# Performance work log

Hardware: AMD Instinct MI355X
Metric: run time of the kernel (lower is better)

Reference implementation:

```python
import jax, jax.numpy as jnp
import numpy as np

Q_HEADS, KV_HEADS, DIMS, IN_DIMS = 16, 4, 1024, 1024
HEAD_D = DIMS // Q_HEADS            # 64
GROUPS = Q_HEADS // KV_HEADS        # 4
ROPE_BASE = 10000.0


def nd_rope(x, coords):
    """N-D rotary embedding.
    x: [..., s, d]; coords: broadcastable [..., s, a] (float).
    Head dim d is split into a contiguous chunks of d//a; within each chunk
    consecutive pairs (2i, 2i+1) are rotated by angle coord_axis * base^(-2i/(d//a)).
    """
    a = coords.shape[-1]
    d = x.shape[-1]
    dpa = d // a                                  # dims per coordinate axis (even)
    inv_freq = ROPE_BASE ** (-jnp.arange(dpa // 2, dtype=jnp.float32) * (2.0 / dpa))
    angles = coords[..., :, None] * inv_freq      # [..., s, a, dpa//2]
    angles = angles.reshape(angles.shape[:-2] + (d // 2,))
    cos, sin = jnp.cos(angles), jnp.sin(angles)
    xp = x.reshape(x.shape[:-1] + (d // 2, 2))
    x1, x2 = xp[..., 0], xp[..., 1]
    return jnp.stack([x1 * cos - x2 * sin, x1 * sin + x2 * cos], axis=-1).reshape(x.shape)


def setup_inputs() -> dict:
    key = jax.random.key(0)
    k1, k2, k3, k4, k5, k6, k7, k8 = jax.random.split(key, 8)
    B, SQ, SKV, A = 4, 2048, 2048, 2
    q = jax.random.normal(k1, (B, SQ, IN_DIMS), dtype=jnp.float32)
    kv = jax.random.normal(k2, (B, SKV, IN_DIMS), dtype=jnp.float32)
    q_coords = jax.random.randint(k3, (B, SQ, A), 0, 2048, dtype=jnp.int32)
    kv_coords = jax.random.randint(k4, (B, SKV, A), 0, 2048, dtype=jnp.int32)
    s_in = 1.0 / np.sqrt(IN_DIMS)
    Wq = jax.random.normal(k5, (IN_DIMS, Q_HEADS, HEAD_D), dtype=jnp.float32) * s_in
    Wk = jax.random.normal(k6, (IN_DIMS, KV_HEADS, HEAD_D), dtype=jnp.float32) * s_in
    Wv = jax.random.normal(k7, (IN_DIMS, KV_HEADS, HEAD_D), dtype=jnp.float32) * s_in
    Wo = jax.random.normal(k8, (KV_HEADS * HEAD_D, IN_DIMS), dtype=jnp.float32) * (1.0 / np.sqrt(KV_HEADS * HEAD_D))
    return {"q": q, "q_coords": q_coords, "kv": kv, "kv_coords": kv_coords,
            "Wq": Wq, "Wk": Wk, "Wv": Wv, "Wo": Wo}


def reference(q, q_coords, kv, kv_coords, Wq, Wk, Wv, Wo):
    B, SQ = q.shape[0], q.shape[1]
    qp = jnp.einsum('bsi,ihd->bshd', q, Wq)   # [b, sq, q_heads, hd]
    kp = jnp.einsum('bsi,ihd->bshd', kv, Wk)  # [b, skv, kv_heads, hd]
    vp = jnp.einsum('bsi,ihd->bshd', kv, Wv)
    # '... s (h g) d -> ... g h s d' with h=KV_HEADS outer, g=GROUPS inner
    qp = qp.reshape(B, SQ, KV_HEADS, GROUPS, HEAD_D).transpose(0, 3, 2, 1, 4)  # [b,g,h,sq,hd]
    kp = kp.transpose(0, 2, 1, 3)  # [b,h,skv,hd]
    vp = vp.transpose(0, 2, 1, 3)
    qc = q_coords.astype(jnp.float32)[:, None, None]  # [b,1,1,sq,a] -> broadcast over g,h
    kc = kv_coords.astype(jnp.float32)[:, None]       # [b,1,skv,a] -> broadcast over h
    qr = nd_rope(qp, qc)
    kr = nd_rope(kp, kc)
    # NOTE: einops pattern omits g in output -> group axis is SUMMED (faithful to source)
    scores = jnp.einsum('bghsd,bhad->bhsa', qr, kr) / (HEAD_D ** 0.5)
    attn = jax.nn.softmax(scores, axis=-1)
    out = jnp.einsum('bhsa,bhad->bhsd', attn, vp)
    out = out.transpose(0, 2, 1, 3).reshape(B, SQ, KV_HEADS * HEAD_D)
    return out @ Wo
```

## Files before the change

### kernel.cpp

```cpp
#include <hip/hip_runtime.h>

#define BATCH 4
#define SEQQ  2048
#define SEQKV 2048
#define NH    4
#define HD    64
#define IND   1024
#define QSCL 0.18033688011112042f

typedef __attribute__((ext_vector_type(8))) short short8;
typedef __attribute__((ext_vector_type(4))) short s4v;
typedef __attribute__((ext_vector_type(4))) float floatx4;

#if defined(__HIP_DEVICE_COMPILE__) && __has_builtin(__builtin_amdgcn_exp2f)
  #define EXP2(x) __builtin_amdgcn_exp2f(x)
#else
  #define EXP2(x) exp2f(x)
#endif

#if defined(__HIP_DEVICE_COMPILE__)
  #if __has_builtin(__builtin_amdgcn_mfma_f32_16x16x16bf16_1k)
    #define MFMA16(a, b, c) __builtin_amdgcn_mfma_f32_16x16x16bf16_1k(a, b, c, 0, 0, 0)
  #elif __has_builtin(__builtin_amdgcn_mfma_f32_16x16x16_bf16)
    #define MFMA16(a, b, c) __builtin_amdgcn_mfma_f32_16x16x16_bf16(a, b, c, 0, 0, 0)
  #else
    #error "no 16x16x16 bf16 MFMA builtin on gfx950 device pass"
  #endif
#else
  #define MFMA16(a, b, c) (c)
#endif
#define MFMA32(a, b, c) __builtin_amdgcn_mfma_f32_16x16x32_bf16(a, b, c, 0, 0, 0)

__device__ __forceinline__ short f2b(float f) {
    unsigned u; __builtin_memcpy(&u, &f, 4);
    u = (u + 0x7fffu + ((u >> 16) & 1u)) >> 16;
    return (short)u;
}
__device__ __forceinline__ short8 cvt8(const float* p) {
    float4 a = *(const float4*)p;
    float4 b = *(const float4*)(p + 4);
    short8 r;
    r[0] = f2b(a.x); r[1] = f2b(a.y); r[2] = f2b(a.z); r[3] = f2b(a.w);
    r[4] = f2b(b.x); r[5] = f2b(b.y); r[6] = f2b(b.z); r[7] = f2b(b.w);
    return r;
}

__global__ __launch_bounds__(256) void prep_all(
    const float* __restrict__ Wq, const float* __restrict__ Wk,
    const float* __restrict__ Wv, const float* __restrict__ Wo,
    const float* __restrict__ q, const float* __restrict__ kv,
    short* __restrict__ Wq_t, short* __restrict__ Wkv_t, short* __restrict__ Wo_t,
    short* __restrict__ qb, short* __restrict__ kvb) {
    __shared__ short Ts[64][65];
    int blk = blockIdx.x;
    if (blk < 256) {
        int c4 = threadIdx.x & 63, r4 = threadIdx.x >> 6;
        if (blk < 64) {
            int h = blk & 3, ib = blk >> 2;
#pragma unroll 4
            for (int jj = 0; jj < 16; ++jj) {
                int il = r4 * 16 + jj;
                float s = 0.f;
#pragma unroll
                for (int g = 0; g < 4; ++g)
                    s += Wq[(ib * 64 + il) * 1024 + (h * 4 + g) * 64 + c4];
                Ts[il][c4] = f2b(s);
            }
            __syncthreads();
#pragma unroll 4
            for (int jj = 0; jj < 16; ++jj) {
                int dl = r4 * 16 + jj;
                Wq_t[(h * 64 + dl) * 1024 + ib * 64 + c4] = Ts[c4][dl];
            }
        } else if (blk < 192) {
            int t = blk - 64, ss = t >> 6; t &= 63;
            int ib = t >> 2, nb = t & 3;
            const float* W = ss ? Wv : Wk;
#pragma unroll 4
            for (int jj = 0; jj < 16; ++jj) {
                int il = r4 * 16 + jj;
                Ts[il][c4] = f2b(W[(ib * 64 + il) * 256 + nb * 64 + c4]);
            }
            __syncthreads();
#pragma unroll 4
            for (int jj = 0; jj < 16; ++jj) {
                int dl = r4 * 16 + jj;
                Wkv_t[(ss * 256 + nb * 64 + dl) * 1024 + ib * 64 + c4] = Ts[c4][dl];
            }
        } else {
            int t = blk - 192, kb = t >> 4, nb = t & 15;
#pragma unroll 4
            for (int jj = 0; jj < 16; ++jj) {
                int il = r4 * 16 + jj;
                Ts[il][c4] = f2b(Wo[(kb * 64 + il) * 1024 + nb * 64 + c4]);
            }
            __syncthreads();
#pragma unroll 4
            for (int jj = 0; jj < 16; ++jj) {
                int dl = r4 * 16 + jj;
                Wo_t[(nb * 64 + dl) * 256 + kb * 64 + c4] = Ts[c4][dl];
            }
        }
    } else if (blk < 2304) {
        long e = ((long)(blk - 256) * 256 + threadIdx.x) * 16;
        *(short8*)(qb + e)     = cvt8(q + e);
        *(short8*)(qb + e + 8) = cvt8(q + e + 8);
    } else {
        long e = ((long)(blk - 2304) * 256 + threadIdx.x) * 16;
        *(short8*)(kvb + e)     = cvt8(kv + e);
        *(short8*)(kvb + e + 8) = cvt8(kv + e + 8);
    }
}

template <int MODE>
__device__ __forceinline__ void gemm128(
    const short* __restrict__ A, const short* __restrict__ Wt,
    int m0, int n0, int N, int K, short* As, short* Bs,
    float* __restrict__ C, const int* __restrict__ coords,
    short* __restrict__ ropeDst, short* __restrict__ vDst) {
    const int t = threadIdx.x;
    const int w = t >> 6, lane = t & 63, ln = lane & 15, quad = lane >> 4;
    const int wm = w >> 1, wn = w & 1;
    const int srow = lane >> 2, skc = (lane & 3) * 8;
    floatx4 acc[4][4];
#pragma unroll
    for (int mt = 0; mt < 4; ++mt)
#pragma unroll
        for (int nt = 0; nt < 4; ++nt) acc[mt][nt] = floatx4{0.f, 0.f, 0.f, 0.f};

    auto stage = [&](int ks, int sel) {
#pragma unroll
        for (int i = 0; i < 2; ++i) {
            __builtin_amdgcn_global_load_lds(
                (const void*)(A + (long)(m0 + w * 32 + i * 16 + srow) * K + ks + skc),
                (void*)(As + sel * 4096 + (w * 2 + i) * 512), 16, 0, 0);
            __builtin_amdgcn_global_load_lds(
                (const void*)(Wt + (long)(n0 + w * 32 + i * 16 + srow) * K + ks + skc),
                (void*)(Bs + sel * 4096 + (w * 2 + i) * 512), 16, 0, 0);
        }
    };

    const int nk = K >> 5;
    stage(0, 0);
    __syncthreads();
    int cur = 0;
    for (int tt = 0; tt < nk; ++tt) {
        if (tt < nk - 1) stage((tt + 1) * 32, cur ^ 1);
        const short* Ac = As + cur * 4096;
        const short* Bc = Bs + cur * 4096;
        short8 af[4], bf[4];
#pragma unroll
        for (int mt = 0; mt < 4; ++mt)
            af[mt] = *(const short8*)(Ac + (wm * 64 + mt * 16 + ln) * 32 + quad * 8);
#pragma unroll
        for (int nt = 0; nt < 4; ++nt)
            bf[nt] = *(const short8*)(Bc + (wn * 64 + nt * 16 + ln) * 32 + quad * 8);
#pragma unroll
        for (int mt = 0; mt < 4; ++mt)
#pragma unroll
            for (int nt = 0; nt < 4; ++nt)
                acc[mt][nt] = MFMA32(af[mt], bf[nt], acc[mt][nt]);
        __syncthreads();
        cur ^= 1;
    }

    if (MODE == 0) {
#pragma unroll
        for (int mt = 0; mt < 4; ++mt) {
            int row0 = m0 + wm * 64 + mt * 16 + quad * 4;
#pragma unroll
            for (int nt = 0; nt < 4; ++nt) {
                int col = n0 + wn * 64 + nt * 16 + ln;
#pragma unroll
                for (int r = 0; r < 4; ++r)
                    C[(long)(row0 + r) * N + col] = acc[mt][nt][r];
            }
        }
    } else {
        const int wn_col = n0 + wn * 64;
        if (MODE == 1 || wn_col < 256) {
            const int h = (wn_col >> 6) & 3;
            const float scl = (MODE == 1) ? QSCL : 1.0f;
            const float L = -0.5756462732485114f;
            const float fA = __expf((float)(ln >> 1) * L);
            const float fB = __expf((float)(8 + (ln >> 1)) * L);
            const float sgn = (ln & 1) ? 1.0f : -1.0f;
#pragma unroll
            for (int mt = 0; mt < 4; ++mt) {
                int row0 = m0 + wm * 64 + mt * 16 + quad * 4;
#pragma unroll
                for (int r = 0; r < 4; ++r) {
                    int row = row0 + r;
                    float c0 = (float)coords[row * 2];
                    float c1 = (float)coords[row * 2 + 1];
                    float snv[4], csv[4];
                    __sincosf(c0 * fA, &snv[0], &csv[0]);
                    __sincosf(c0 * fB, &snv[1], &csv[1]);
                    __sincosf(c1 * fA, &snv[2], &csv[2]);
                    __sincosf(c1 * fB, &snv[3], &csv[3]);
                    long rbase = ((long)((row >> 11) * 4 + h) * 2048 + (row & 2047)) * 64;
#pragma unroll
                    for (int nt = 0; nt < 4; ++nt) {
                        float v = acc[mt][nt][r];
                        float p = __shfl_xor(v, 1, 64);
                        float o = v * (csv[nt] * scl) + p * (snv[nt] * (scl * sgn));
                        ropeDst[rbase + nt * 16 + ln] = f2b(o);
                    }
                }
            }
        } else {
            const int h = ((wn_col - 256) >> 6) & 3;
#pragma unroll
            for (int mt = 0; mt < 4; ++mt) {
                int row0 = m0 + wm * 64 + mt * 16 + quad * 4;
                int b = row0 >> 11, s0 = row0 & 2047;
#pragma unroll
                for (int nt = 0; nt < 4; ++nt) {
                    s4v ov;
#pragma unroll
                    for (int r = 0; r < 4; ++r) ov[r] = f2b(acc[mt][nt][r]);
                    *(s4v*)(vDst + (long)((b * 4 + h) * 64 + nt * 16 + ln) * 2048 + s0) = ov;
                }
            }
        }
    }
}

__global__ __launch_bounds__(256) void proj_gemm(
    const short* __restrict__ qb, const short* __restrict__ kvb,
    const short* __restrict__ Wq_t, const short* __restrict__ Wkv_t,
    const int* __restrict__ qc, const int* __restrict__ kvc,
    short* __restrict__ Qr, short* __restrict__ Kr, short* __restrict__ Vt) {
    __shared__ __align__(16) short As[2][128 * 32];
    __shared__ __align__(16) short Bs[2][128 * 32];
    int id = blockIdx.x;
    if (id < 128)
        gemm128<1>(qb, Wq_t, (id >> 1) * 128, (id & 1) * 128, 256, 1024,
                   &As[0][0], &Bs[0][0], nullptr, qc, Qr, nullptr);
    else {
        int t = id - 128;
        gemm128<2>(kvb, Wkv_t, (t >> 2) * 128, (t & 3) * 128, 512, 1024,
                   &As[0][0], &Bs[0][0], nullptr, kvc, Kr, Vt);
    }
}

__global__ __launch_bounds__(256) void final_gemm(
    const short* __restrict__ Ob, const short* __restrict__ Wo_t, float* __restrict__ out) {
    __shared__ __align__(16) short As[2][128 * 32];
    __shared__ __align__(16) short Bs[2][128 * 32];
    gemm128<0>(Ob, Wo_t, blockIdx.x * 128, blockIdx.y * 128, 1024, 256,
               &As[0][0], &Bs[0][0], out, nullptr, nullptr, nullptr);
}

__global__ __launch_bounds__(256, 4) void attn_kernel(
    const short* __restrict__ Qr, const short* __restrict__ Kr,
    const short* __restrict__ Vt, float* __restrict__ Op, float* __restrict__ Lp) {
    __shared__ __align__(16) short Kls[2][64 * 64];
    __shared__ __align__(16) short Vls[2][64 * 64];
    const int blk = blockIdx.x;
    const int bh = blk & 15, sp = (blk >> 4) & 3, qg = blk >> 6;
    const int w = threadIdx.x >> 6, lane = threadIdx.x & 63;
    const int ln = lane & 15, quad = lane >> 4;
    const int q0 = qg * 128 + w * 32;
    const short* Qb = Qr + (long)bh * SEQKV * HD;
    const short* Kb = Kr + (long)bh * SEQKV * HD;
    const short* Vb = Vt + (long)bh * HD * SEQKV;

    const int srow = lane >> 3;
    const int schk = (lane & 7) ^ (srow & 7);
    const long kstage0 = (long)(w * 16 + srow) * HD + schk * 8;
    const long vstage0 = (long)(w * 16 + srow) * SEQKV + schk * 8;

    short8 qf[2][2];
#pragma unroll
    for (int qs = 0; qs < 2; ++qs)
#pragma unroll
        for (int ck = 0; ck < 2; ++ck)
            qf[qs][ck] = *(const short8*)(Qb + (long)(q0 + qs * 16 + ln) * HD + ck * 32 + quad * 8);

    s4v ones;
#pragma unroll
    for (int j = 0; j < 4; ++j) ones[j] = (short)0x3F80;

    floatx4 o[2][4], ol[2];
#pragma unroll
    for (int qs = 0; qs < 2; ++qs) {
        ol[qs] = floatx4{0.f, 0.f, 0.f, 0.f};
#pragma unroll
        for (int nt = 0; nt < 4; ++nt) o[qs][nt] = floatx4{0.f, 0.f, 0.f, 0.f};
    }

    const int ln7 = ln & 7;
    int koff[2];
#pragma unroll
    for (int ck = 0; ck < 2; ++ck) koff[ck] = ln * 64 + ((ck * 4 + quad) ^ ln7) * 8;
    int voff[4];
#pragma unroll
    for (int t = 0; t < 4; ++t) voff[t] = ln * 64 + ((t * 2 + (quad >> 1)) ^ ln7) * 8 + (quad & 1) * 4;

    const int kt0 = sp * 512;
#define STAGE(kt, sel)                                                              \
    do {                                                                            \
        _Pragma("unroll")                                                           \
        for (int i = 0; i < 2; ++i) {                                               \
            __builtin_amdgcn_global_load_lds(                                       \
                (const void*)(Kb + (long)(kt) * HD + kstage0 + (long)i * 8 * HD),   \
                (void*)(Kls[sel] + (w * 16 + i * 8) * 64), 16, 0, 0);               \
            __builtin_amdgcn_global_load_lds(                                       \
                (const void*)(Vb + (kt) + vstage0 + (long)i * 8 * SEQKV),           \
                (void*)(Vls[sel] + (w * 16 + i * 8) * 64), 16, 0, 0);               \
        }                                                                           \
    } while (0)

    STAGE(kt0, 0);
    __syncthreads();
    int cur = 0;
    for (int tt = 0; tt < 8; ++tt) {
        if (tt < 7) STAGE(kt0 + (tt + 1) * 64, cur ^ 1);
        const short* Kc = Kls[cur];
        const short* Vc = Vls[cur];
#pragma unroll
        for (int t = 0; t < 4; ++t) {
            short8 a0 = *(const short8*)(Kc + t * 1024 + koff[0]);
            short8 a1 = *(const short8*)(Kc + t * 1024 + koff[1]);
            floatx4 st0 = {0.f, 0.f, 0.f, 0.f}, st1 = {0.f, 0.f, 0.f, 0.f};
            __builtin_amdgcn_s_setprio(1);
            st0 = MFMA32(a0, qf[0][0], st0);
            st1 = MFMA32(a0, qf[1][0], st1);
            st0 = MFMA32(a1, qf[0][1], st0);
            st1 = MFMA32(a1, qf[1][1], st1);
            __builtin_amdgcn_s_setprio(0);
            float e0 = EXP2(st0[0]), e1 = EXP2(st0[1]), e2 = EXP2(st0[2]), e3 = EXP2(st0[3]);
            float g0 = EXP2(st1[0]), g1 = EXP2(st1[1]), g2 = EXP2(st1[2]), g3 = EXP2(st1[3]);
            unsigned a0p, a1p, b0p, b1p;
            asm("v_cvt_pk_bf16_f32 %0, %1, %2" : "=v"(a0p) : "v"(e0), "v"(e1));
            asm("v_cvt_pk_bf16_f32 %0, %1, %2" : "=v"(a1p) : "v"(e2), "v"(e3));
            asm("v_cvt_pk_bf16_f32 %0, %1, %2" : "=v"(b0p) : "v"(g0), "v"(g1));
            asm("v_cvt_pk_bf16_f32 %0, %1, %2" : "=v"(b1p) : "v"(g2), "v"(g3));
            s4v pt0, pt1;
            { unsigned tmp[2] = {a0p, a1p}; __builtin_memcpy(&pt0, tmp, 8); }
            { unsigned tmp[2] = {b0p, b1p}; __builtin_memcpy(&pt1, tmp, 8); }
            __builtin_amdgcn_s_setprio(1);
#pragma unroll
            for (int nt = 0; nt < 4; ++nt) {
                s4v vf = *(const s4v*)(Vc + nt * 1024 + voff[t]);
                o[0][nt] = MFMA16(vf, pt0, o[0][nt]);
                o[1][nt] = MFMA16(vf, pt1, o[1][nt]);
            }
            ol[0] = MFMA16(ones, pt0, ol[0]);
            ol[1] = MFMA16(ones, pt1, ol[1]);
            __builtin_amdgcn_s_setprio(0);
        }
        __syncthreads();
        cur ^= 1;
    }
#undef STAGE
#pragma unroll
    for (int qs = 0; qs < 2; ++qs) {
        long qrow = (long)(sp * 16 + bh) * 2048 + q0 + qs * 16 + ln;
        if (quad == 0) Lp[qrow] = ol[qs][0];
#pragma unroll
        for (int nt = 0; nt < 4; ++nt)
            *(floatx4*)(Op + qrow * 64 + nt * 16 + quad * 4) = o[qs][nt];
    }
}

__global__ __launch_bounds__(256) void combine_kernel(
    const float* __restrict__ Op, const float* __restrict__ Lp, short* __restrict__ Ob) {
    int idx = blockIdx.x * 256 + threadIdx.x;
    int row = idx >> 4;
    int d0 = (idx & 15) * 4;
    int bh = row >> 11, qq = row & 2047;
    int b = bh >> 2, h = bh & 3;
    float4 os = {0.f, 0.f, 0.f, 0.f};
    float ls = 0.f;
#pragma unroll
    for (int s = 0; s < 4; ++s) {
        long rr = (long)(s * 16 + bh) * 2048 + qq;
        float4 v = *(const float4*)(Op + rr * 64 + d0);
        os.x += v.x; os.y += v.y; os.z += v.z; os.w += v.w;
        ls += Lp[rr];
    }
    float li = 1.f / ls;
    s4v ov;
    ov[0] = f2b(os.x * li); ov[1] = f2b(os.y * li);
    ov[2] = f2b(os.z * li); ov[3] = f2b(os.w * li);
    *(s4v*)(Ob + ((long)(b * 2048 + qq)) * 256 + h * 64 + d0) = ov;
}

extern "C" void kernel_launch(void* const* d_in, const int* in_sizes, int n_in,
                              void* d_out, int out_size, void* d_ws, size_t ws_size,
                              hipStream_t stream) {
    const float* q   = (const float*)d_in[0];
    const int*   qc  = (const int*)d_in[1];
    const float* kv  = (const float*)d_in[2];
    const int*   kvc = (const int*)d_in[3];
    const float* Wq  = (const float*)d_in[4];
    const float* Wk  = (const float*)d_in[5];
    const float* Wv  = (const float*)d_in[6];
    const float* Wo  = (const float*)d_in[7];
    float* out = (float*)d_out;

    char* ws = (char*)d_ws;
    const size_t MB = 1024 * 1024;
    short* Wq_t  = (short*)(ws);
    short* Wkv_t = (short*)(ws + MB / 2);
    short* Wo_t  = (short*)(ws + 3 * MB / 2);
    short* qb    = (short*)(ws + 2 * MB);
    short* kvb   = (short*)(ws + 18 * MB);
    short* Qr    = (short*)(ws + 34 * MB);
    short* Kr    = (short*)(ws + 38 * MB);
    short* Vt    = (short*)(ws + 42 * MB);
    short* Ob    = (short*)(ws + 46 * MB);
    float* Opart = (float*)(ws + 50 * MB);
    float* Lpart = (float*)(ws + 82 * MB);

    hipLaunchKernelGGL(prep_all, dim3(4352), dim3(256), 0, stream,
                       Wq, Wk, Wv, Wo, q, kv, Wq_t, Wkv_t, Wo_t, qb, kvb);
    hipLaunchKernelGGL(proj_gemm, dim3(384), dim3(256), 0, stream,
                       qb, kvb, Wq_t, Wkv_t, qc, kvc, Qr, Kr, Vt);
    hipLaunchKernelGGL(attn_kernel, dim3(1024), dim3(256), 0, stream,
                       Qr, Kr, Vt, Opart, Lpart);
    hipLaunchKernelGGL(combine_kernel, dim3(2048), dim3(256), 0, stream,
                       Opart, Lpart, Ob);
    hipLaunchKernelGGL(final_gemm, dim3(64, 8), dim3(256), 0, stream, Ob, Wo_t, out);
}
```

Baseline: 193.6 us.

## Fuse fp32 input conversion into projection GEMM and drop split-KV attention combine

The projection GEMM now stages the fp32 q/kv activations into LDS with an XOR swizzle and converts them to bf16 in registers. This removes the separate conversion pass that wrote bf16 copies of the inputs. The attention kernel no longer splits the KV range four ways. Each block covers 64 queries over the full 2048 keys, normalises in-kernel and writes bf16 output directly, which eliminates the partial-sum buffers and the combine kernel. The trade-offs are half as many attention blocks (512) with a longer serial loop, and a larger fp32 LDS footprint in the projection.

Measured after the change: 209.5 us. +8.2%, slower.

```diff
diff --git a/kernel.cpp b/kernel.cpp
--- a/kernel.cpp
+++ b/kernel.cpp
@@ -36,92 +36,73 @@
     u = (u + 0x7fffu + ((u >> 16) & 1u)) >> 16;
     return (short)u;
 }
-__device__ __forceinline__ short8 cvt8(const float* p) {
-    float4 a = *(const float4*)p;
-    float4 b = *(const float4*)(p + 4);
-    short8 r;
-    r[0] = f2b(a.x); r[1] = f2b(a.y); r[2] = f2b(a.z); r[3] = f2b(a.w);
-    r[4] = f2b(b.x); r[5] = f2b(b.y); r[6] = f2b(b.z); r[7] = f2b(b.w);
-    return r;
-}
-
-__global__ __launch_bounds__(256) void prep_all(
+
+__global__ __launch_bounds__(256) void prep_w(
     const float* __restrict__ Wq, const float* __restrict__ Wk,
     const float* __restrict__ Wv, const float* __restrict__ Wo,
-    const float* __restrict__ q, const float* __restrict__ kv,
-    short* __restrict__ Wq_t, short* __restrict__ Wkv_t, short* __restrict__ Wo_t,
-    short* __restrict__ qb, short* __restrict__ kvb) {
+    short* __restrict__ Wq_t, short* __restrict__ Wkv_t, short* __restrict__ Wo_t) {
     __shared__ short Ts[64][65];
     int blk = blockIdx.x;
-    if (blk < 256) {
-        int c4 = threadIdx.x & 63, r4 = threadIdx.x >> 6;
-        if (blk < 64) {
-            int h = blk & 3, ib = blk >> 2;
-#pragma unroll 4
-            for (int jj = 0; jj < 16; ++jj) {
-                int il = r4 * 16 + jj;
-                float s = 0.f;
-#pragma unroll
-                for (int g = 0; g < 4; ++g)
-                    s += Wq[(ib * 64 + il) * 1024 + (h * 4 + g) * 64 + c4];
-                Ts[il][c4] = f2b(s);
-            }
-            __syncthreads();
-#pragma unroll 4
-            for (int jj = 0; jj < 16; ++jj) {
-                int dl = r4 * 16 + jj;
-                Wq_t[(h * 64 + dl) * 1024 + ib * 64 + c4] = Ts[c4][dl];
-            }
-        } else if (blk < 192) {
-            int t = blk - 64, ss = t >> 6; t &= 63;
-            int ib = t >> 2, nb = t & 3;
-            const float* W = ss ? Wv : Wk;
-#pragma unroll 4
-            for (int jj = 0; jj < 16; ++jj) {
-                int il = r4 * 16 + jj;
-                Ts[il][c4] = f2b(W[(ib * 64 + il) * 256 + nb * 64 + c4]);
-            }
-            __syncthreads();
-#pragma unroll 4
-            for (int jj = 0; jj < 16; ++jj) {
-                int dl = r4 * 16 + jj;
-                Wkv_t[(ss * 256 + nb * 64 + dl) * 1024 + ib * 64 + c4] = Ts[c4][dl];
-            }
-        } else {
-            int t = blk - 192, kb = t >> 4, nb = t & 15;
-#pragma unroll 4
-            for (int jj = 0; jj < 16; ++jj) {
-                int il = r4 * 16 + jj;
-                Ts[il][c4] = f2b(Wo[(kb * 64 + il) * 1024 + nb * 64 + c4]);
-            }
-            __syncthreads();
-#pragma unroll 4
-            for (int jj = 0; jj < 16; ++jj) {
-                int dl = r4 * 16 + jj;
-                Wo_t[(nb * 64 + dl) * 256 + kb * 64 + c4] = Ts[c4][dl];
-            }
-        }
-    } else if (blk < 2304) {
-        long e = ((long)(blk - 256) * 256 + threadIdx.x) * 16;
-        *(short8*)(qb + e)     = cvt8(q + e);
-        *(short8*)(qb + e + 8) = cvt8(q + e + 8);
+    int c4 = threadIdx.x & 63, r4 = threadIdx.x >> 6;
+    if (blk < 64) {
+        int h = blk & 3, ib = blk >> 2;
+#pragma unroll 4
+        for (int jj = 0; jj < 16; ++jj) {
+            int il = r4 * 16 + jj;
+            float s = 0.f;
+#pragma unroll
+            for (int g = 0; g < 4; ++g)
+                s += Wq[(ib * 64 + il) * 1024 + (h * 4 + g) * 64 + c4];
+            Ts[il][c4] = f2b(s);
+        }
+        __syncthreads();
+#pragma unroll 4
+        for (int jj = 0; jj < 16; ++jj) {
+            int dl = r4 * 16 + jj;
+            Wq_t[(h * 64 + dl) * 1024 + ib * 64 + c4] = Ts[c4][dl];
+        }
+    } else if (blk < 192) {
+        int t = blk - 64, ss = t >> 6; t &= 63;
+        int ib = t >> 2, nb = t & 3;
+        const float* W = ss ? Wv : Wk;
+#pragma unroll 4
+        for (int jj = 0; jj < 16; ++jj) {
+            int il = r4 * 16 + jj;
+            Ts[il][c4] = f2b(W[(ib * 64 + il) * 256 + nb * 64 + c4]);
+        }
+        __syncthreads();
+#pragma unroll 4
+        for (int jj = 0; jj < 16; ++jj) {
+            int dl = r4 * 16 + jj;
+            Wkv_t[(ss * 256 + nb * 64 + dl) * 1024 + ib * 64 + c4] = Ts[c4][dl];
+        }
     } else {
-        long e = ((long)(blk - 2304) * 256 + threadIdx.x) * 16;
-        *(short8*)(kvb + e)     = cvt8(kv + e);
-        *(short8*)(kvb + e + 8) = cvt8(kv + e + 8);
+        int t = blk - 192, kb = t >> 4, nb = t & 15;
+#pragma unroll 4
+        for (int jj = 0; jj < 16; ++jj) {
+            int il = r4 * 16 + jj;
+            Ts[il][c4] = f2b(Wo[(kb * 64 + il) * 1024 + nb * 64 + c4]);
+        }
+        __syncthreads();
+#pragma unroll 4
+        for (int jj = 0; jj < 16; ++jj) {
+            int dl = r4 * 16 + jj;
+            Wo_t[(nb * 64 + dl) * 256 + kb * 64 + c4] = Ts[c4][dl];
+        }
     }
 }
 
 template <int MODE>
-__device__ __forceinline__ void gemm128(
-    const short* __restrict__ A, const short* __restrict__ Wt,
-    int m0, int n0, int N, int K, short* As, short* Bs,
-    float* __restrict__ C, const int* __restrict__ coords,
-    short* __restrict__ ropeDst, short* __restrict__ vDst) {
-    const int t = threadIdx.x;
-    const int w = t >> 6, lane = t & 63, ln = lane & 15, quad = lane >> 4;
+__device__ __forceinline__ void gemm128_f32(
+    const float* __restrict__ A, const short* __restrict__ Wt,
+    int m0, int n0, int K, float* Asf, short* Bs,
+    const int* __restrict__ coords, short* __restrict__ ropeDst,
+    short* __restrict__ vDst) {
+    const int tid = threadIdx.x;
+    const int w = tid >> 6, lane = tid & 63, ln = lane & 15, quad = lane >> 4;
     const int wm = w >> 1, wn = w & 1;
-    const int srow = lane >> 2, skc = (lane & 3) * 8;
+    const int srowA = lane >> 3, schkA = (lane & 7) ^ (srowA & 7);
+    const int srowB = lane >> 2, skcB = (lane & 3) * 8;
     floatx4 acc[4][4];
 #pragma unroll
     for (int mt = 0; mt < 4; ++mt)
@@ -130,14 +111,15 @@
 
     auto stage = [&](int ks, int sel) {
 #pragma unroll
-        for (int i = 0; i < 2; ++i) {
+        for (int i = 0; i < 4; ++i)
             __builtin_amdgcn_global_load_lds(
-                (const void*)(A + (long)(m0 + w * 32 + i * 16 + srow) * K + ks + skc),
-                (void*)(As + sel * 4096 + (w * 2 + i) * 512), 16, 0, 0);
+                (const void*)(A + (long)(m0 + w * 32 + i * 8 + srowA) * 1024 + ks + schkA * 4),
+                (void*)(Asf + sel * 4096 + (w * 32 + i * 8) * 32), 16, 0, 0);
+#pragma unroll
+        for (int i = 0; i < 2; ++i)
             __builtin_amdgcn_global_load_lds(
-                (const void*)(Wt + (long)(n0 + w * 32 + i * 16 + srow) * K + ks + skc),
+                (const void*)(Wt + (long)(n0 + w * 32 + i * 16 + srowB) * K + ks + skcB),
                 (void*)(Bs + sel * 4096 + (w * 2 + i) * 512), 16, 0, 0);
-        }
     };
 
     const int nk = K >> 5;
@@ -146,12 +128,23 @@
     int cur = 0;
     for (int tt = 0; tt < nk; ++tt) {
         if (tt < nk - 1) stage((tt + 1) * 32, cur ^ 1);
-        const short* Ac = As + cur * 4096;
+        const float* Ac = Asf + cur * 4096;
         const short* Bc = Bs + cur * 4096;
+        const int e = ln & 7;
         short8 af[4], bf[4];
 #pragma unroll
-        for (int mt = 0; mt < 4; ++mt)
-            af[mt] = *(const short8*)(Ac + (wm * 64 + mt * 16 + ln) * 32 + quad * 8);
+        for (int mt = 0; mt < 4; ++mt) {
+            const float* rp = Ac + (wm * 64 + mt * 16 + ln) * 32;
+            float4 lo = *(const float4*)(rp + ((2 * quad) ^ e) * 4);
+            float4 hi = *(const float4*)(rp + ((2 * quad + 1) ^ e) * 4);
+            unsigned p0, p1, p2, p3;
+            asm("v_cvt_pk_bf16_f32 %0, %1, %2" : "=v"(p0) : "v"(lo.x), "v"(lo.y));
+            asm("v_cvt_pk_bf16_f32 %0, %1, %2" : "=v"(p1) : "v"(lo.z), "v"(lo.w));
+            asm("v_cvt_pk_bf16_f32 %0, %1, %2" : "=v"(p2) : "v"(hi.x), "v"(hi.y));
+            asm("v_cvt_pk_bf16_f32 %0, %1, %2" : "=v"(p3) : "v"(hi.z), "v"(hi.w));
+            unsigned tmp[4] = {p0, p1, p2, p3};
+            __builtin_memcpy(&af[mt], tmp, 16);
+        }
 #pragma unroll
         for (int nt = 0; nt < 4; ++nt)
             bf[nt] = *(const short8*)(Bc + (wn * 64 + nt * 16 + ln) * 32 + quad * 8);
@@ -164,83 +157,69 @@
         cur ^= 1;
     }
 
-    if (MODE == 0) {
+    const int wn_col = n0 + wn * 64;
+    if (MODE == 1 || wn_col < 256) {
+        const int h = (wn_col >> 6) & 3;
+        const float scl = (MODE == 1) ? QSCL : 1.0f;
+        const float L = -0.5756462732485114f;
+        const float fA = __expf((float)(ln >> 1) * L);
+        const float fB = __expf((float)(8 + (ln >> 1)) * L);
+        const float sgn = (ln & 1) ? 1.0f : -1.0f;
 #pragma unroll
         for (int mt = 0; mt < 4; ++mt) {
             int row0 = m0 + wm * 64 + mt * 16 + quad * 4;
 #pragma unroll
-            for (int nt = 0; nt < 4; ++nt) {
-                int col = n0 + wn * 64 + nt * 16 + ln;
-#pragma unroll
-                for (int r = 0; r < 4; ++r)
-                    C[(long)(row0 + r) * N + col] = acc[mt][nt][r];
-            }
-        }
-    } else {
-        const int wn_col = n0 + wn * 64;
-        if (MODE == 1 || wn_col < 256) {
-            const int h = (wn_col >> 6) & 3;
-            const float scl = (MODE == 1) ? QSCL : 1.0f;
-            const float L = -0.5756462732485114f;
-            const float fA = __expf((float)(ln >> 1) * L);
-            const float fB = __expf((float)(8 + (ln >> 1)) * L);
-            const float sgn = (ln & 1) ? 1.0f : -1.0f;
-#pragma unroll
-            for (int mt = 0; mt < 4; ++mt) {
-                int row0 = m0 + wm * 64 + mt * 16 + quad * 4;
-#pragma unroll
-                for (int r = 0; r < 4; ++r) {
-                    int row = row0 + r;
-                    float c0 = (float)coords[row * 2];
-                    float c1 = (float)coords[row * 2 + 1];
-                    float snv[4], csv[4];
-                    __sincosf(c0 * fA, &snv[0], &csv[0]);
-                    __sincosf(c0 * fB, &snv[1], &csv[1]);
-                    __sincosf(c1 * fA, &snv[2], &csv[2]);
-                    __sincosf(c1 * fB, &snv[3], &csv[3]);
-                    long rbase = ((long)((row >> 11) * 4 + h) * 2048 + (row & 2047)) * 64;
-#pragma unroll
-                    for (int nt = 0; nt < 4; ++nt) {
-                        float v = acc[mt][nt][r];
-                        float p = __shfl_xor(v, 1, 64);
-                        float o = v * (csv[nt] * scl) + p * (snv[nt] * (scl * sgn));
-                        ropeDst[rbase + nt * 16 + ln] = f2b(o);
-                    }
+            for (int r = 0; r < 4; ++r) {
+                int row = row0 + r;
+                float c0 = (float)coords[row * 2];
+                float c1 = (float)coords[row * 2 + 1];
+                float snv[4], csv[4];
+                __sincosf(c0 * fA, &snv[0], &csv[0]);
+                __sincosf(c0 * fB, &snv[1], &csv[1]);
+                __sincosf(c1 * fA, &snv[2], &csv[2]);
+                __sincosf(c1 * fB, &snv[3], &csv[3]);
+                long rbase = ((long)((row >> 11) * 4 + h) * 2048 + (row & 2047)) * 64;
+#pragma unroll
+                for (int nt = 0; nt < 4; ++nt) {
+                    float v = acc[mt][nt][r];
+                    float p = __shfl_xor(v, 1, 64);
+                    float o = v * (csv[nt] * scl) + p * (snv[nt] * (scl * sgn));
+                    ropeDst[rbase + nt * 16 + ln] = f2b(o);
                 }
             }
-        } else {
-            const int h = ((wn_col - 256) >> 6) & 3;
-#pragma unroll
-            for (int mt = 0; mt < 4; ++mt) {
-                int row0 = m0 + wm * 64 + mt * 16 + quad * 4;
-                int b = row0 >> 11, s0 = row0 & 2047;
-#pragma unroll
-                for (int nt = 0; nt < 4; ++nt) {
-                    s4v ov;
-#pragma unroll
-                    for (int r = 0; r < 4; ++r) ov[r] = f2b(acc[mt][nt][r]);
-                    *(s4v*)(vDst + (long)((b * 4 + h) * 64 + nt * 16 + ln) * 2048 + s0) = ov;
-                }
+        }
+    } else {
+        const int h = ((wn_col - 256) >> 6) & 3;
+#pragma unroll
+        for (int mt = 0; mt < 4; ++mt) {
+            int row0 = m0 + wm * 64 + mt * 16 + quad * 4;
+            int b = row0 >> 11, s0 = row0 & 2047;
+#pragma unroll
+            for (int nt = 0; nt < 4; ++nt) {
+                s4v ov;
+#pragma unroll
+                for (int r = 0; r < 4; ++r) ov[r] = f2b(acc[mt][nt][r]);
+                *(s4v*)(vDst + (long)((b * 4 + h) * 64 + nt * 16 + ln) * 2048 + s0) = ov;
             }
         }
     }
 }
 
 __global__ __launch_bounds__(256) void proj_gemm(
-    const short* __restrict__ qb, const short* __restrict__ kvb,
+    const float* __restrict__ q, const float* __restrict__ kv,
     const short* __restrict__ Wq_t, const short* __restrict__ Wkv_t,
     const int* __restrict__ qc, const int* __restrict__ kvc,
     short* __restrict__ Qr, short* __restrict__ Kr, short* __restrict__ Vt) {
-    __shared__ __align__(16) short As[2][128 * 32];
-    __shared__ __align__(16) short Bs[2][128 * 32];
+    __shared__ __align__(16) float Asf[2 * 4096];
+    __shared__ __align__(16) short Bsb[2 * 4096];
     int id = blockIdx.x;
     if (id < 128)
-        gemm128<1>(qb, Wq_t, (id >> 1) * 128, (id & 1) * 128, 256, 1024,
-                   &As[0][0], &Bs[0][0], nullptr, qc, Qr, nullptr);
+        gemm128_f32<1>(q, Wq_t, (id >> 1) * 128, (id & 1) * 128, 1024,
+                       Asf, Bsb, qc, Qr, nullptr);
     else {
         int t = id - 128;
-        gemm128<2>(kvb, Wkv_t, (t >> 2) * 128, (t & 3) * 128, 512, 1024,
-                   &As[0][0], &Bs[0][0], nullptr, kvc, Kr, Vt);
+        gemm128_f32<2>(kv, Wkv_t, (t >> 2) * 128, (t & 3) * 128, 1024,
+                       Asf, Bsb, kvc, Kr, Vt);
     }
 }
 
@@ -248,20 +227,74 @@
     const short* __restrict__ Ob, const short* __restrict__ Wo_t, float* __restrict__ out) {
     __shared__ __align__(16) short As[2][128 * 32];
     __shared__ __align__(16) short Bs[2][128 * 32];
-    gemm128<0>(Ob, Wo_t, blockIdx.x * 128, blockIdx.y * 128, 1024, 256,
-               &As[0][0], &Bs[0][0], out, nullptr, nullptr, nullptr);
+    const int m0 = blockIdx.x * 128, n0 = blockIdx.y * 128;
+    const int tid = threadIdx.x;
+    const int w = tid >> 6, lane = tid & 63, ln = lane & 15, quad = lane >> 4;
+    const int wm = w >> 1, wn = w & 1;
+    const int srow = lane >> 2, skc = (lane & 3) * 8;
+    floatx4 acc[4][4];
+#pragma unroll
+    for (int mt = 0; mt < 4; ++mt)
+#pragma unroll
+        for (int nt = 0; nt < 4; ++nt) acc[mt][nt] = floatx4{0.f, 0.f, 0.f, 0.f};
+
+    auto stage = [&](int ks, int sel) {
+#pragma unroll
+        for (int i = 0; i < 2; ++i) {
+            __builtin_amdgcn_global_load_lds(
+                (const void*)(Ob + (long)(m0 + w * 32 + i * 16 + srow) * 256 + ks + skc),
+                (void*)(&As[sel][(w * 2 + i) * 512]), 16, 0, 0);
+            __builtin_amdgcn_global_load_lds(
+                (const void*)(Wo_t + (long)(n0 + w * 32 + i * 16 + srow) * 256 + ks + skc),
+                (void*)(&Bs[sel][(w * 2 + i) * 512]), 16, 0, 0);
+        }
+    };
+    stage(0, 0);
+    __syncthreads();
+    int cur = 0;
+    for (int tt = 0; tt < 8; ++tt) {
+        if (tt < 7) stage((tt + 1) * 32, cur ^ 1);
+        const short* Ac = &As[cur][0];
+        const short* Bc = &Bs[cur][0];
+        short8 af[4], bf[4];
+#pragma unroll
+        for (int mt = 0; mt < 4; ++mt)
+            af[mt] = *(const short8*)(Ac + (wm * 64 + mt * 16 + ln) * 32 + quad * 8);
+#pragma unroll
+        for (int nt = 0; nt < 4; ++nt)
+            bf[nt] = *(const short8*)(Bc + (wn * 64 + nt * 16 + ln) * 32 + quad * 8);
+#pragma unroll
+        for (int mt = 0; mt < 4; ++mt)
+#pragma unroll
+            for (int nt = 0; nt < 4; ++nt)
+                acc[mt][nt] = MFMA32(af[mt], bf[nt], acc[mt][nt]);
+        __syncthreads();
+        cur ^= 1;
+    }
+#pragma unroll
+    for (int mt = 0; mt < 4; ++mt) {
+        int row0 = m0 + wm * 64 + mt * 16 + quad * 4;
+#pragma unroll
+        for (int nt = 0; nt < 4; ++nt) {
+            int col = n0 + wn * 64 + nt * 16 + ln;
+#pragma unroll
+            for (int r = 0; r < 4; ++r)
+                out[(long)(row0 + r) * 1024 + col] = acc[mt][nt][r];
+        }
+    }
 }
 
 __global__ __launch_bounds__(256, 4) void attn_kernel(
     const short* __restrict__ Qr, const short* __restrict__ Kr,
-    const short* __restrict__ Vt, float* __restrict__ Op, float* __restrict__ Lp) {
+    const short* __restrict__ Vt, short* __restrict__ Ob) {
     __shared__ __align__(16) short Kls[2][64 * 64];
     __shared__ __align__(16) short Vls[2][64 * 64];
     const int blk = blockIdx.x;
-    const int bh = blk & 15, sp = (blk >> 4) & 3, qg = blk >> 6;
+    const int x = blk & 7, y = blk >> 3;
+    const int bh = x * 2 + (y >> 5), qg = y & 31;
     const int w = threadIdx.x >> 6, lane = threadIdx.x & 63;
     const int ln = lane & 15, quad = lane >> 4;
-    const int q0 = qg * 128 + w * 32;
+    const int q0 = qg * 64 + w * 16;
     const short* Qb = Qr + (long)bh * SEQKV * HD;
     const short* Kb = Kr + (long)bh * SEQKV * HD;
     const short* Vb = Vt + (long)bh * HD * SEQKV;
@@ -271,24 +304,19 @@
     const long kstage0 = (long)(w * 16 + srow) * HD + schk * 8;
     const long vstage0 = (long)(w * 16 + srow) * SEQKV + schk * 8;
 
-    short8 qf[2][2];
-#pragma unroll
-    for (int qs = 0; qs < 2; ++qs)
-#pragma unroll
-        for (int ck = 0; ck < 2; ++ck)
-            qf[qs][ck] = *(const short8*)(Qb + (long)(q0 + qs * 16 + ln) * HD + ck * 32 + quad * 8);
+    short8 qf[2];
+#pragma unroll
+    for (int ck = 0; ck < 2; ++ck)
+        qf[ck] = *(const short8*)(Qb + (long)(q0 + ln) * HD + ck * 32 + quad * 8);
 
     s4v ones;
 #pragma unroll
     for (int j = 0; j < 4; ++j) ones[j] = (short)0x3F80;
 
-    floatx4 o[2][4], ol[2];
-#pragma unroll
-    for (int qs = 0; qs < 2; ++qs) {
-        ol[qs] = floatx4{0.f, 0.f, 0.f, 0.f};
-#pragma unroll
-        for (int nt = 0; nt < 4; ++nt) o[qs][nt] = floatx4{0.f, 0.f, 0.f, 0.f};
-    }
+    floatx4 o[4], ol;
+    ol = floatx4{0.f, 0.f, 0.f, 0.f};
+#pragma unroll
+    for (int nt = 0; nt < 4; ++nt) o[nt] = floatx4{0.f, 0.f, 0.f, 0.f};
 
     const int ln7 = ln & 7;
     int koff[2];
@@ -298,94 +326,64 @@
 #pragma unroll
     for (int t = 0; t < 4; ++t) voff[t] = ln * 64 + ((t * 2 + (quad >> 1)) ^ ln7) * 8 + (quad & 1) * 4;
 
-    const int kt0 = sp * 512;
 #define STAGE(kt, sel)                                                              \
     do {                                                                            \
         _Pragma("unroll")                                                           \
         for (int i = 0; i < 2; ++i) {                                               \
             __builtin_amdgcn_global_load_lds(                                       \
                 (const void*)(Kb + (long)(kt) * HD + kstage0 + (long)i * 8 * HD),   \
-                (void*)(Kls[sel] + (w * 16 + i * 8) * 64), 16, 0, 0);               \
+                (void*)(&Kls[sel][(w * 16 + i * 8) * 64]), 16, 0, 0);               \
             __builtin_amdgcn_global_load_lds(                                       \
                 (const void*)(Vb + (kt) + vstage0 + (long)i * 8 * SEQKV),           \
-                (void*)(Vls[sel] + (w * 16 + i * 8) * 64), 16, 0, 0);               \
+                (void*)(&Vls[sel][(w * 16 + i * 8) * 64]), 16, 0, 0);               \
         }                                                                           \
     } while (0)
 
-    STAGE(kt0, 0);
+    STAGE(0, 0);
     __syncthreads();
     int cur = 0;
-    for (int tt = 0; tt < 8; ++tt) {
-        if (tt < 7) STAGE(kt0 + (tt + 1) * 64, cur ^ 1);
-        const short* Kc = Kls[cur];
-        const short* Vc = Vls[cur];
+    for (int tt = 0; tt < 32; ++tt) {
+        if (tt < 31) STAGE((tt + 1) * 64, cur ^ 1);
+        const short* Kc = &Kls[cur][0];
+        const short* Vc = &Vls[cur][0];
 #pragma unroll
         for (int t = 0; t < 4; ++t) {
             short8 a0 = *(const short8*)(Kc + t * 1024 + koff[0]);
             short8 a1 = *(const short8*)(Kc + t * 1024 + koff[1]);
-            floatx4 st0 = {0.f, 0.f, 0.f, 0.f}, st1 = {0.f, 0.f, 0.f, 0.f};
+            floatx4 st = {0.f, 0.f, 0.f, 0.f};
             __builtin_amdgcn_s_setprio(1);
-            st0 = MFMA32(a0, qf[0][0], st0);
-            st1 = MFMA32(a0, qf[1][0], st1);
-            st0 = MFMA32(a1, qf[0][1], st0);
-            st1 = MFMA32(a1, qf[1][1], st1);
+            st = MFMA32(a0, qf[0], st);
+            st = MFMA32(a1, qf[1], st);
             __builtin_amdgcn_s_setprio(0);
-            float e0 = EXP2(st0[0]), e1 = EXP2(st0[1]), e2 = EXP2(st0[2]), e3 = EXP2(st0[3]);
-            float g0 = EXP2(st1[0]), g1 = EXP2(st1[1]), g2 = EXP2(st1[2]), g3 = EXP2(st1[3]);
-            unsigned a0p, a1p, b0p, b1p;
-            asm("v_cvt_pk_bf16_f32 %0, %1, %2" : "=v"(a0p) : "v"(e0), "v"(e1));
-            asm("v_cvt_pk_bf16_f32 %0, %1, %2" : "=v"(a1p) : "v"(e2), "v"(e3));
-            asm("v_cvt_pk_bf16_f32 %0, %1, %2" : "=v"(b0p) : "v"(g0), "v"(g1));
-            asm("v_cvt_pk_bf16_f32 %0, %1, %2" : "=v"(b1p) : "v"(g2), "v"(g3));
-            s4v pt0, pt1;
-            { unsigned tmp[2] = {a0p, a1p}; __builtin_memcpy(&pt0, tmp, 8); }
-            { unsigned tmp[2] = {b0p, b1p}; __builtin_memcpy(&pt1, tmp, 8); }
+            float e0 = EXP2(st[0]), e1 = EXP2(st[1]), e2 = EXP2(st[2]), e3 = EXP2(st[3]);
+            unsigned p0, p1;
+            asm("v_cvt_pk_bf16_f32 %0, %1, %2" : "=v"(p0) : "v"(e0), "v"(e1));
+            asm("v_cvt_pk_bf16_f32 %0, %1, %2" : "=v"(p1) : "v"(e2), "v"(e3));
+            s4v pt;
+            { unsigned tmp[2] = {p0, p1}; __builtin_memcpy(&pt, tmp, 8); }
             __builtin_amdgcn_s_setprio(1);
 #pragma unroll
             for (int nt = 0; nt < 4; ++nt) {
                 s4v vf = *(const s4v*)(Vc + nt * 1024 + voff[t]);
-                o[0][nt] = MFMA16(vf, pt0, o[0][nt]);
-                o[1][nt] = MFMA16(vf, pt1, o[1][nt]);
+                o[nt] = MFMA16(vf, pt, o[nt]);
             }
-            ol[0] = MFMA16(ones, pt0, ol[0]);
-            ol[1] = MFMA16(ones, pt1, ol[1]);
+            ol = MFMA16(ones, pt, ol);
             __builtin_amdgcn_s_setprio(0);
         }
         __syncthreads();
         cur ^= 1;
     }
 #undef STAGE
-#pragma unroll
-    for (int qs = 0; qs < 2; ++qs) {
-        long qrow = (long)(sp * 16 + bh) * 2048 + q0 + qs * 16 + ln;
-        if (quad == 0) Lp[qrow] = ol[qs][0];
-#pragma unroll
-        for (int nt = 0; nt < 4; ++nt)
-            *(floatx4*)(Op + qrow * 64 + nt * 16 + quad * 4) = o[qs][nt];
-    }
-}
-
-__global__ __launch_bounds__(256) void combine_kernel(
-    const float* __restrict__ Op, const float* __restrict__ Lp, short* __restrict__ Ob) {
-    int idx = blockIdx.x * 256 + threadIdx.x;
-    int row = idx >> 4;
-    int d0 = (idx & 15) * 4;
-    int bh = row >> 11, qq = row & 2047;
-    int b = bh >> 2, h = bh & 3;
-    float4 os = {0.f, 0.f, 0.f, 0.f};
-    float ls = 0.f;
-#pragma unroll
-    for (int s = 0; s < 4; ++s) {
-        long rr = (long)(s * 16 + bh) * 2048 + qq;
-        float4 v = *(const float4*)(Op + rr * 64 + d0);
-        os.x += v.x; os.y += v.y; os.z += v.z; os.w += v.w;
-        ls += Lp[rr];
-    }
-    float li = 1.f / ls;
-    s4v ov;
-    ov[0] = f2b(os.x * li); ov[1] = f2b(os.y * li);
-    ov[2] = f2b(os.z * li); ov[3] = f2b(os.w * li);
-    *(s4v*)(Ob + ((long)(b * 2048 + qq)) * 256 + h * 64 + d0) = ov;
+    const int b = bh >> 2, h = bh & 3;
+    const float li = 1.0f / ol[0];
+    const long base = ((long)(b * 2048 + q0 + ln)) * 256 + h * 64;
+#pragma unroll
+    for (int nt = 0; nt < 4; ++nt) {
+        s4v ov;
+#pragma unroll
+        for (int r = 0; r < 4; ++r) ov[r] = f2b(o[nt][r] * li);
+        *(s4v*)(Ob + base + nt * 16 + quad * 4) = ov;
+    }
 }
 
 extern "C" void kernel_launch(void* const* d_in, const int* in_sizes, int n_in,
@@ -406,22 +404,16 @@
     short* Wq_t  = (short*)(ws);
     short* Wkv_t = (short*)(ws + MB / 2);
     short* Wo_t  = (short*)(ws + 3 * MB / 2);
-    short* qb    = (short*)(ws + 2 * MB);
-    short* kvb   = (short*)(ws + 18 * MB);
-    short* Qr    = (short*)(ws + 34 * MB);
-    short* Kr    = (short*)(ws + 38 * MB);
-    short* Vt    = (short*)(ws + 42 * MB);
-    short* Ob    = (short*)(ws + 46 * MB);
-    float* Opart = (float*)(ws + 50 * MB);
-    float* Lpart = (float*)(ws + 82 * MB);
-
-    hipLaunchKernelGGL(prep_all, dim3(4352), dim3(256), 0, stream,
-                       Wq, Wk, Wv, Wo, q, kv, Wq_t, Wkv_t, Wo_t, qb, kvb);
+    short* Qr    = (short*)(ws + 2 * MB);
+    short* Kr    = (short*)(ws + 6 * MB);
+    short* Vt    = (short*)(ws + 10 * MB);
+    short* Ob    = (short*)(ws + 14 * MB);
+
+    hipLaunchKernelGGL(prep_w, dim3(256), dim3(256), 0, stream,
+                       Wq, Wk, Wv, Wo, Wq_t, Wkv_t, Wo_t);
     hipLaunchKernelGGL(proj_gemm, dim3(384), dim3(256), 0, stream,
-                       qb, kvb, Wq_t, Wkv_t, qc, kvc, Qr, Kr, Vt);
-    hipLaunchKernelGGL(attn_kernel, dim3(1024), dim3(256), 0, stream,
-                       Qr, Kr, Vt, Opart, Lpart);
-    hipLaunchKernelGGL(combine_kernel, dim3(2048), dim3(256), 0, stream,
-                       Opart, Lpart, Ob);
+                       q, kv, Wq_t, Wkv_t, qc, kvc, Qr, Kr, Vt);
+    hipLaunchKernelGGL(attn_kernel, dim3(512), dim3(256), 0, stream,
+                       Qr, Kr, Vt, Ob);
     hipLaunchKernelGGL(final_gemm, dim3(64, 8), dim3(256), 0, stream, Ob, Wo_t, out);
 }
```

## Drop split-KV attention and fuse normalization into attention epilogue

Applied to the files above, without the earlier changes.

Each attention block now walks the full KV sequence for 64 query rows (16 per wave) instead of a quarter of KV for 128 rows. The softmax denominator is applied in the epilogue, which writes bf16 output directly. This removes the combine kernel and the fp32 partial-output and partial-sum buffers along with their round trip through memory. In exchange the grid is halved to 512 blocks, each wave covers fewer query rows, and every K/V tile loaded into LDS is reused across fewer queries, which lowers occupancy and reuse.

Measured after the change: 203.0 us. 1.05x slower.

```diff
diff --git a/kernel.cpp b/kernel.cpp
--- a/kernel.cpp
+++ b/kernel.cpp
@@ -254,14 +254,15 @@
 
 __global__ __launch_bounds__(256, 4) void attn_kernel(
     const short* __restrict__ Qr, const short* __restrict__ Kr,
-    const short* __restrict__ Vt, float* __restrict__ Op, float* __restrict__ Lp) {
+    const short* __restrict__ Vt, short* __restrict__ Ob) {
     __shared__ __align__(16) short Kls[2][64 * 64];
     __shared__ __align__(16) short Vls[2][64 * 64];
     const int blk = blockIdx.x;
-    const int bh = blk & 15, sp = (blk >> 4) & 3, qg = blk >> 6;
+    const int x = blk & 7, y = blk >> 3;
+    const int bh = x * 2 + (y >> 5), qg = y & 31;
     const int w = threadIdx.x >> 6, lane = threadIdx.x & 63;
     const int ln = lane & 15, quad = lane >> 4;
-    const int q0 = qg * 128 + w * 32;
+    const int q0 = qg * 64 + w * 16;
     const short* Qb = Qr + (long)bh * SEQKV * HD;
     const short* Kb = Kr + (long)bh * SEQKV * HD;
     const short* Vb = Vt + (long)bh * HD * SEQKV;
@@ -271,24 +272,19 @@
     const long kstage0 = (long)(w * 16 + srow) * HD + schk * 8;
     const long vstage0 = (long)(w * 16 + srow) * SEQKV + schk * 8;
 
-    short8 qf[2][2];
-#pragma unroll
-    for (int qs = 0; qs < 2; ++qs)
-#pragma unroll
-        for (int ck = 0; ck < 2; ++ck)
-            qf[qs][ck] = *(const short8*)(Qb + (long)(q0 + qs * 16 + ln) * HD + ck * 32 + quad * 8);
+    short8 qf[2];
+#pragma unroll
+    for (int ck = 0; ck < 2; ++ck)
+        qf[ck] = *(const short8*)(Qb + (long)(q0 + ln) * HD + ck * 32 + quad * 8);
 
     s4v ones;
 #pragma unroll
     for (int j = 0; j < 4; ++j) ones[j] = (short)0x3F80;
 
-    floatx4 o[2][4], ol[2];
-#pragma unroll
-    for (int qs = 0; qs < 2; ++qs) {
-        ol[qs] = floatx4{0.f, 0.f, 0.f, 0.f};
-#pragma unroll
-        for (int nt = 0; nt < 4; ++nt) o[qs][nt] = floatx4{0.f, 0.f, 0.f, 0.f};
-    }
+    floatx4 o[4], ol;
+    ol = floatx4{0.f, 0.f, 0.f, 0.f};
+#pragma unroll
+    for (int nt = 0; nt < 4; ++nt) o[nt] = floatx4{0.f, 0.f, 0.f, 0.f};
 
     const int ln7 = ln & 7;
     int koff[2];
@@ -298,94 +294,64 @@
 #pragma unroll
     for (int t = 0; t < 4; ++t) voff[t] = ln * 64 + ((t * 2 + (quad >> 1)) ^ ln7) * 8 + (quad & 1) * 4;
 
-    const int kt0 = sp * 512;
 #define STAGE(kt, sel)                                                              \
     do {                                                                            \
         _Pragma("unroll")                                                           \
         for (int i = 0; i < 2; ++i) {                                               \
             __builtin_amdgcn_global_load_lds(                                       \
                 (const void*)(Kb + (long)(kt) * HD + kstage0 + (long)i * 8 * HD),   \
-                (void*)(Kls[sel] + (w * 16 + i * 8) * 64), 16, 0, 0);               \
+                (void*)(&Kls[sel][(w * 16 + i * 8) * 64]), 16, 0, 0);               \
             __builtin_amdgcn_global_load_lds(                                       \
                 (const void*)(Vb + (kt) + vstage0 + (long)i * 8 * SEQKV),           \
-                (void*)(Vls[sel] + (w * 16 + i * 8) * 64), 16, 0, 0);               \
+                (void*)(&Vls[sel][(w * 16 + i * 8) * 64]), 16, 0, 0);               \
         }                                                                           \
     } while (0)
 
-    STAGE(kt0, 0);
+    STAGE(0, 0);
     __syncthreads();
     int cur = 0;
-    for (int tt = 0; tt < 8; ++tt) {
-        if (tt < 7) STAGE(kt0 + (tt + 1) * 64, cur ^ 1);
-        const short* Kc = Kls[cur];
-        const short* Vc = Vls[cur];
+    for (int tt = 0; tt < 32; ++tt) {
+        if (tt < 31) STAGE((tt + 1) * 64, cur ^ 1);
+        const short* Kc = &Kls[cur][0];
+        const short* Vc = &Vls[cur][0];
 #pragma unroll
         for (int t = 0; t < 4; ++t) {
             short8 a0 = *(const short8*)(Kc + t * 1024 + koff[0]);
             short8 a1 = *(const short8*)(Kc + t * 1024 + koff[1]);
-            floatx4 st0 = {0.f, 0.f, 0.f, 0.f}, st1 = {0.f, 0.f, 0.f, 0.f};
+            floatx4 st = {0.f, 0.f, 0.f, 0.f};
             __builtin_amdgcn_s_setprio(1);
-            st0 = MFMA32(a0, qf[0][0], st0);
-            st1 = MFMA32(a0, qf[1][0], st1);
-            st0 = MFMA32(a1, qf[0][1], st0);
-            st1 = MFMA32(a1, qf[1][1], st1);
+            st = MFMA32(a0, qf[0], st);
+            st = MFMA32(a1, qf[1], st);
             __builtin_amdgcn_s_setprio(0);
-            float e0 = EXP2(st0[0]), e1 = EXP2(st0[1]), e2 = EXP2(st0[2]), e3 = EXP2(st0[3]);
-            float g0 = EXP2(st1[0]), g1 = EXP2(st1[1]), g2 = EXP2(st1[2]), g3 = EXP2(st1[3]);
-            unsigned a0p, a1p, b0p, b1p;
-            asm("v_cvt_pk_bf16_f32 %0, %1, %2" : "=v"(a0p) : "v"(e0), "v"(e1));
-            asm("v_cvt_pk_bf16_f32 %0, %1, %2" : "=v"(a1p) : "v"(e2), "v"(e3));
-            asm("v_cvt_pk_bf16_f32 %0, %1, %2" : "=v"(b0p) : "v"(g0), "v"(g1));
-            asm("v_cvt_pk_bf16_f32 %0, %1, %2" : "=v"(b1p) : "v"(g2), "v"(g3));
-            s4v pt0, pt1;
-            { unsigned tmp[2] = {a0p, a1p}; __builtin_memcpy(&pt0, tmp, 8); }
-            { unsigned tmp[2] = {b0p, b1p}; __builtin_memcpy(&pt1, tmp, 8); }
+            float e0 = EXP2(st[0]), e1 = EXP2(st[1]), e2 = EXP2(st[2]), e3 = EXP2(st[3]);
+            unsigned p0, p1;
+            asm("v_cvt_pk_bf16_f32 %0, %1, %2" : "=v"(p0) : "v"(e0), "v"(e1));
+            asm("v_cvt_pk_bf16_f32 %0, %1, %2" : "=v"(p1) : "v"(e2), "v"(e3));
+            s4v pt;
+            { unsigned tmp[2] = {p0, p1}; __builtin_memcpy(&pt, tmp, 8); }
             __builtin_amdgcn_s_setprio(1);
 #pragma unroll
             for (int nt = 0; nt < 4; ++nt) {
                 s4v vf = *(const s4v*)(Vc + nt * 1024 + voff[t]);
-                o[0][nt] = MFMA16(vf, pt0, o[0][nt]);
-                o[1][nt] = MFMA16(vf, pt1, o[1][nt]);
-            }
-            ol[0] = MFMA16(ones, pt0, ol[0]);
-            ol[1] = MFMA16(ones, pt1, ol[1]);
+                o[nt] = MFMA16(vf, pt, o[nt]);
+            }
+            ol = MFMA16(ones, pt, ol);
             __builtin_amdgcn_s_setprio(0);
         }
         __syncthreads();
         cur ^= 1;
     }
 #undef STAGE
-#pragma unroll
-    for (int qs = 0; qs < 2; ++qs) {
-        long qrow = (long)(sp * 16 + bh) * 2048 + q0 + qs * 16 + ln;
-        if (quad == 0) Lp[qrow] = ol[qs][0];
-#pragma unroll
-        for (int nt = 0; nt < 4; ++nt)
-            *(floatx4*)(Op + qrow * 64 + nt * 16 + quad * 4) = o[qs][nt];
-    }
-}
-
-__global__ __launch_bounds__(256) void combine_kernel(
-    const float* __restrict__ Op, const float* __restrict__ Lp, short* __restrict__ Ob) {
-    int idx = blockIdx.x * 256 + threadIdx.x;
-    int row = idx >> 4;
-    int d0 = (idx & 15) * 4;
-    int bh = row >> 11, qq = row & 2047;
-    int b = bh >> 2, h = bh & 3;
-    float4 os = {0.f, 0.f, 0.f, 0.f};
-    float ls = 0.f;
-#pragma unroll
-    for (int s = 0; s < 4; ++s) {
-        long rr = (long)(s * 16 + bh) * 2048 + qq;
-        float4 v = *(const float4*)(Op + rr * 64 + d0);
-        os.x += v.x; os.y += v.y; os.z += v.z; os.w += v.w;
-        ls += Lp[rr];
-    }
-    float li = 1.f / ls;
-    s4v ov;
-    ov[0] = f2b(os.x * li); ov[1] = f2b(os.y * li);
-    ov[2] = f2b(os.z * li); ov[3] = f2b(os.w * li);
-    *(s4v*)(Ob + ((long)(b * 2048 + qq)) * 256 + h * 64 + d0) = ov;
+    const int b = bh >> 2, h = bh & 3;
+    const float li = 1.0f / ol[0];
+    const long base = ((long)(b * 2048 + q0 + ln)) * 256 + h * 64;
+#pragma unroll
+    for (int nt = 0; nt < 4; ++nt) {
+        s4v ov;
+#pragma unroll
+        for (int r = 0; r < 4; ++r) ov[r] = f2b(o[nt][r] * li);
+        *(s4v*)(Ob + base + nt * 16 + quad * 4) = ov;
+    }
 }
 
 extern "C" void kernel_launch(void* const* d_in, const int* in_sizes, int n_in,
@@ -412,16 +378,12 @@
     short* Kr    = (short*)(ws + 38 * MB);
     short* Vt    = (short*)(ws + 42 * MB);
     short* Ob    = (short*)(ws + 46 * MB);
-    float* Opart = (float*)(ws + 50 * MB);
-    float* Lpart = (float*)(ws + 82 * MB);
 
     hipLaunchKernelGGL(prep_all, dim3(4352), dim3(256), 0, stream,
                        Wq, Wk, Wv, Wo, q, kv, Wq_t, Wkv_t, Wo_t, qb, kvb);
     hipLaunchKernelGGL(proj_gemm, dim3(384), dim3(256), 0, stream,
                        qb, kvb, Wq_t, Wkv_t, qc, kvc, Qr, Kr, Vt);
-    hipLaunchKernelGGL(attn_kernel, dim3(1024), dim3(256), 0, stream,
-                       Qr, Kr, Vt, Opart, Lpart);
-    hipLaunchKernelGGL(combine_kernel, dim3(2048), dim3(256), 0, stream,
-                       Opart, Lpart, Ob);
+    hipLaunchKernelGGL(attn_kernel, dim3(512), dim3(256), 0, stream,
+                       Qr, Kr, Vt, Ob);
     hipLaunchKernelGGL(final_gemm, dim3(64, 8), dim3(256), 0, stream, Ob, Wo_t, out);
 }
```
